# Optimization experiments

Measured on AMD Instinct MI355X. Metric: run time of the kernel, lower is better.

## Reference

```python
import jax, jax.numpy as jnp
import numpy as np

N_NODES = 50000
N_EDGES = 600000
IC, H, OC = 64, 128, 32
EPS = 1e-5


def setup_inputs() -> dict:
    key = jax.random.key(0)
    ks = jax.random.split(key, 8)
    x = jax.random.normal(ks[0], (N_NODES, IC), dtype=jnp.float32)
    ei = jax.random.randint(ks[1], (2, N_EDGES), 0, N_NODES, dtype=jnp.int64)
    proj_w = jax.random.normal(ks[2], (IC, H), dtype=jnp.float32) * 0.05
    proj_b = jnp.zeros((H,), dtype=jnp.float32)
    # conv_w[layer, lin, :, :] with lin order: key, query, value, skip
    conv_w = jax.random.normal(ks[3], (3, 4, H, H), dtype=jnp.float32) * 0.05
    conv_b = jnp.zeros((3, 4, H), dtype=jnp.float32)
    bn_gamma = jnp.ones((3, H), dtype=jnp.float32)
    bn_beta = jnp.zeros((3, H), dtype=jnp.float32)
    head_w = jax.random.normal(ks[4], (H, OC), dtype=jnp.float32) * 0.05
    head_b = jnp.zeros((OC,), dtype=jnp.float32)
    return {"x": x, "ei": ei, "proj_w": proj_w, "proj_b": proj_b,
            "conv_w": conv_w, "conv_b": conv_b, "bn_gamma": bn_gamma,
            "bn_beta": bn_beta, "head_w": head_w, "head_b": head_b}


def _res_gated_conv(x, src, dst, w, b):
    # PyG ResGatedGraphConv: out_i = skip(x_i) + sum_j sigmoid(key(x_i)+query(x_j)) * value(x_j)
    k = x @ w[0] + b[0]      # key   (applied to target/dst)
    q = x @ w[1] + b[1]      # query (applied to source/src)
    v = x @ w[2] + b[2]      # value (applied to source/src)
    msg = jax.nn.sigmoid(k[dst] + q[src]) * v[src]          # [E, H]
    agg = jax.ops.segment_sum(msg, dst, num_segments=x.shape[0])  # [N, H]
    return x @ w[3] + b[3] + agg


def _batchnorm(x, gamma, beta):
    # training-mode BatchNorm1d: batch statistics over the node dimension
    mean = jnp.mean(x, axis=0)
    var = jnp.var(x, axis=0)
    return gamma * (x - mean) * jax.lax.rsqrt(var + EPS) + beta


def reference(x, ei, proj_w, proj_b, conv_w, conv_b, bn_gamma, bn_beta, head_w, head_b):
    src, dst = ei[0], ei[1]
    h = jax.nn.relu(x @ proj_w + proj_b)
    for layer in range(3):
        h = _res_gated_conv(h, src, dst, conv_w[layer], conv_b[layer])
        h = jax.nn.relu(_batchnorm(h, bn_gamma[layer], bn_beta[layer]))
        # dropout(p=0.2) is identity in eval mode
    return h @ head_w + head_b
```

## Files before the change

kernel.cpp:

```cpp
#include <hip/hip_runtime.h>
#include <hip/hip_bf16.h>
#include <math.h>

#define HDIM 128
#define ICDIM 64
#define OCDIM 32
#define BN_EPS 1e-5f
#define NCH 64

typedef __attribute__((ext_vector_type(8))) short bv8;
typedef __attribute__((ext_vector_type(4))) float fv4;

static __device__ __forceinline__ unsigned short f2bf(float v) {
    __hip_bfloat16 t = __float2bfloat16(v);
    return *(unsigned short*)&t;
}
static __device__ __forceinline__ float bflo(unsigned int u) {
    union { unsigned int i; float f; } c; c.i = u << 16; return c.f;
}
static __device__ __forceinline__ float bfhi(unsigned int u) {
    union { unsigned int i; float f; } c; c.i = u & 0xffff0000u; return c.f;
}
static __device__ __forceinline__ unsigned int pack2bf(float a, float b) {
    return (unsigned int)f2bf(a) | ((unsigned int)f2bf(b) << 16);
}

__global__ void wprep_kernel(const float* __restrict__ conv_w,
                             const float* __restrict__ proj_w,
                             __hip_bfloat16* __restrict__ Wt,
                             __hip_bfloat16* __restrict__ Wp) {
    int mat = blockIdx.x;
    if (mat < 12) {
        const float* s = conv_w + (size_t)mat * HDIM * HDIM;
        __hip_bfloat16* d = Wt + (size_t)mat * HDIM * HDIM;
        for (int idx = threadIdx.x; idx < HDIM * HDIM; idx += 256) {
            int i = idx >> 7, o = idx & 127;
            d[(size_t)o * HDIM + i] = __float2bfloat16(s[idx]);
        }
    } else {
        for (int idx = threadIdx.x; idx < ICDIM * HDIM; idx += 256) {
            int i = idx >> 7, o = idx & 127;
            Wp[(size_t)o * ICDIM + i] = __float2bfloat16(proj_w[idx]);
        }
    }
}

__global__ __launch_bounds__(256)
void proj_mfma_kernel(const float* __restrict__ x,
                      const __hip_bfloat16* __restrict__ wp,
                      const float* __restrict__ b,
                      __hip_bfloat16* __restrict__ h, int n) {
    __shared__ unsigned int xs[NCH * ICDIM / 2];
    int tid = threadIdx.x;
    int m0 = blockIdx.x * NCH;

    const float2* xsrc = (const float2*)(x + (size_t)m0 * ICDIM);
    for (int i = tid; i < NCH * ICDIM / 2; i += 256) {
        int node = m0 + (i >> 5);
        float2 v = (node < n) ? xsrc[i] : (float2){0.f, 0.f};
        xs[i ^ (((i >> 5) & 7) << 2)] = pack2bf(v.x, v.y);
    }

    int wv = tid >> 6;
    int lane = tid & 63;
    int j = lane & 15;
    int kg = lane >> 4;
    int sw = (j & 7) << 4;

    bv8 af[2][2];
#pragma unroll
    for (int gs = 0; gs < 2; ++gs)
#pragma unroll
        for (int ks = 0; ks < 2; ++ks)
            af[gs][ks] = *(const bv8*)((const unsigned short*)wp +
                (size_t)(wv * 32 + gs * 16 + j) * ICDIM + ks * 32 + kg * 8);

    float4 bias0 = *(const float4*)(b + wv * 32 + kg * 4);
    float4 bias1 = *(const float4*)(b + wv * 32 + 16 + kg * 4);

    __syncthreads();

#pragma unroll
    for (int t4 = 0; t4 < NCH / 16; ++t4) {
        const char* rowbase = (const char*)xs + (t4 * 16 + j) * (ICDIM * 2);
        fv4 acc0 = (fv4){0.f, 0.f, 0.f, 0.f};
        fv4 acc1 = (fv4){0.f, 0.f, 0.f, 0.f};
#pragma unroll
        for (int ks = 0; ks < 2; ++ks) {
            bv8 bf = *(const bv8*)(rowbase + ((kg * 16 + ks * 64) ^ sw));
            acc0 = __builtin_amdgcn_mfma_f32_16x16x32_bf16(af[0][ks], bf, acc0, 0, 0, 0);
            acc1 = __builtin_amdgcn_mfma_f32_16x16x32_bf16(af[1][ks], bf, acc1, 0, 0, 0);
        }
        int node = m0 + t4 * 16 + j;
        if (node < n) {
            unsigned short* o =
                (unsigned short*)h + (size_t)node * HDIM + wv * 32 + kg * 4;
            ushort4 r0, r1;
            r0.x = f2bf(fmaxf(acc0.x + bias0.x, 0.f));
            r0.y = f2bf(fmaxf(acc0.y + bias0.y, 0.f));
            r0.z = f2bf(fmaxf(acc0.z + bias0.z, 0.f));
            r0.w = f2bf(fmaxf(acc0.w + bias0.w, 0.f));
            r1.x = f2bf(fmaxf(acc1.x + bias1.x, 0.f));
            r1.y = f2bf(fmaxf(acc1.y + bias1.y, 0.f));
            r1.z = f2bf(fmaxf(acc1.z + bias1.z, 0.f));
            r1.w = f2bf(fmaxf(acc1.w + bias1.w, 0.f));
            *(ushort4*)o = r0;
            *(ushort4*)(o + 16) = r1;
        }
    }
}

__global__ __launch_bounds__(1024)
void gemm4_fused_kernel(const __hip_bfloat16* __restrict__ hB,
                        const float* __restrict__ Ssrc,
                        const float* __restrict__ stp,
                        const float* __restrict__ gma,
                        const float* __restrict__ bta,
                        const __hip_bfloat16* __restrict__ wt4,
                        const float* __restrict__ b4,
                        __hip_bfloat16* __restrict__ K,
                        unsigned int* __restrict__ QV,
                        float* __restrict__ S, int n) {
    __shared__ unsigned short hs[NCH * HDIM];
    int tid = threadIdx.x;
    int m0 = blockIdx.x * NCH;
    int wsw = ((tid >> 4) & 7) << 4;

    if (Ssrc) {
        const float4* src = (const float4*)(Ssrc + (size_t)m0 * HDIM);
        float4 v0 = src[tid * 2];
        float4 v1 = src[tid * 2 + 1];
        int c0 = (tid * 8) & 127;
        float invn = 1.f / (float)n;
        float vv[8] = {v0.x, v0.y, v0.z, v0.w, v1.x, v1.y, v1.z, v1.w};
        unsigned int* dst = (unsigned int*)((char*)hs + ((tid * 16) ^ wsw));
#pragma unroll
        for (int p = 0; p < 8; p += 2) {
            int c = c0 + p;
            float mA = stp[c] * invn, mB = stp[c + 1] * invn;
            float scA = gma[c] * rsqrtf(stp[128 + c] * invn - mA * mA + BN_EPS);
            float scB = gma[c + 1] * rsqrtf(stp[129 + c] * invn - mB * mB + BN_EPS);
            float shA = bta[c] - mA * scA, shB = bta[c + 1] - mB * scB;
            float rA = fmaxf(fmaf(vv[p], scA, shA), 0.f);
            float rB = fmaxf(fmaf(vv[p + 1], scB, shB), 0.f);
            dst[p >> 1] = pack2bf(rA, rB);
        }
    } else {
        const uint4* src = (const uint4*)((const unsigned short*)hB + (size_t)m0 * HDIM);
        *(uint4*)((char*)hs + ((tid * 16) ^ wsw)) = src[tid];
    }

    int wv = tid >> 6;
    int lane = tid & 63;
    int lin = wv >> 2;
    int g2 = wv & 3;
    int j = lane & 15;
    int kg = lane >> 4;
    int sw = (j & 7) << 4;

    const unsigned short* wbase =
        (const unsigned short*)(wt4 + (size_t)lin * HDIM * HDIM);
    bv8 af[2][4];
#pragma unroll
    for (int gs = 0; gs < 2; ++gs)
#pragma unroll
        for (int ks = 0; ks < 4; ++ks)
            af[gs][ks] = *(const bv8*)(wbase +
                (size_t)(g2 * 32 + gs * 16 + j) * HDIM + ks * 32 + kg * 8);

    const float* bl = b4 + lin * HDIM;
    float4 bias0 = *(const float4*)(bl + g2 * 32 + kg * 4);
    float4 bias1 = *(const float4*)(bl + g2 * 32 + 16 + kg * 4);

    __syncthreads();

#pragma unroll
    for (int t4 = 0; t4 < NCH / 16; ++t4) {
        const char* rowbase = (const char*)hs + (t4 * 16 + j) * (HDIM * 2);
        fv4 acc0 = (fv4){0.f, 0.f, 0.f, 0.f};
        fv4 acc1 = (fv4){0.f, 0.f, 0.f, 0.f};
#pragma unroll
        for (int ks = 0; ks < 4; ++ks) {
            bv8 bf = *(const bv8*)(rowbase + ((kg * 16 + ks * 64) ^ sw));
            acc0 = __builtin_amdgcn_mfma_f32_16x16x32_bf16(af[0][ks], bf, acc0, 0, 0, 0);
            acc1 = __builtin_amdgcn_mfma_f32_16x16x32_bf16(af[1][ks], bf, acc1, 0, 0, 0);
        }
        int node = m0 + t4 * 16 + j;
        if (node >= n) continue;
        int c0 = g2 * 32 + kg * 4;
        float f0 = acc0.x + bias0.x, f1 = acc0.y + bias0.y;
        float f2 = acc0.z + bias0.z, f3 = acc0.w + bias0.w;
        float f4 = acc1.x + bias1.x, f5 = acc1.y + bias1.y;
        float f6 = acc1.z + bias1.z, f7 = acc1.w + bias1.w;
        if (lin == 3) {
            float* o = S + (size_t)node * HDIM + c0;
            *(float4*)o = (float4){f0, f1, f2, f3};
            *(float4*)(o + 16) = (float4){f4, f5, f6, f7};
        } else if (lin == 0) {
            unsigned short* o = (unsigned short*)K + (size_t)node * HDIM + c0;
            *(ushort4*)o = (ushort4){f2bf(f0), f2bf(f1), f2bf(f2), f2bf(f3)};
            *(ushort4*)(o + 16) = (ushort4){f2bf(f4), f2bf(f5), f2bf(f6), f2bf(f7)};
        } else {
            unsigned short* o = (unsigned short*)QV + (size_t)node * 256 + 2 * c0
                              + ((lin == 2) ? 4 : 0);
            *(ushort4*)o = (ushort4){f2bf(f0), f2bf(f1), f2bf(f2), f2bf(f3)};
            *(ushort4*)(o + 32) = (ushort4){f2bf(f4), f2bf(f5), f2bf(f6), f2bf(f7)};
        }
    }
}

__global__ void hist_kernel(const int* __restrict__ ei, int* __restrict__ deg, int e) {
    int i = blockIdx.x * 256 + threadIdx.x;
    if (i < e) atomicAdd(&deg[ei[(size_t)e + i]], 1);
}

__global__ void scan1_kernel(const int* __restrict__ deg, int* __restrict__ incl,
                             int* __restrict__ bsum, int n) {
    __shared__ int tmp[256];
    int i = blockIdx.x * 256 + threadIdx.x;
    int v = (i < n) ? deg[i] : 0;
    tmp[threadIdx.x] = v;
    __syncthreads();
    for (int ofs = 1; ofs < 256; ofs <<= 1) {
        int t = (threadIdx.x >= ofs) ? tmp[threadIdx.x - ofs] : 0;
        __syncthreads();
        tmp[threadIdx.x] += t;
        __syncthreads();
    }
    if (i < n) incl[i] = tmp[threadIdx.x];
    if (threadIdx.x == 255) bsum[blockIdx.x] = tmp[255];
}

__global__ void scan23_kernel(const int* __restrict__ deg, const int* __restrict__ incl,
                              const int* __restrict__ bsum, int* __restrict__ off,
                              int* __restrict__ cursor, int n, int e, int nb) {
    __shared__ int tmp[256];
    int t = threadIdx.x;
    tmp[t] = (t < nb) ? bsum[t] : 0;
    __syncthreads();
    for (int ofs = 1; ofs < 256; ofs <<= 1) {
        int a = (t >= ofs) ? tmp[t - ofs] : 0;
        __syncthreads();
        tmp[t] += a;
        __syncthreads();
    }
    int pre = (blockIdx.x == 0) ? 0 : tmp[blockIdx.x - 1];
    int i = blockIdx.x * 256 + t;
    if (i < n) {
        int ex = incl[i] - deg[i] + pre;
        off[i] = ex;
        cursor[i] = ex;
        if (i == n - 1) off[n] = e;
    }
}

__global__ void scatter_kernel(const int* __restrict__ ei, int* __restrict__ cursor,
                               int* __restrict__ esrc, int e) {
    int i = blockIdx.x * 256 + threadIdx.x;
    if (i < e) {
        int dst = ei[(size_t)e + i];
        int pos = atomicAdd(&cursor[dst], 1);
        esrc[pos] = ei[i];
    }
}

__global__ void agg_kernel(const int* __restrict__ off, const int* __restrict__ esrc,
                           const __hip_bfloat16* __restrict__ kb,
                           const unsigned int* __restrict__ QV,
                           float* __restrict__ S, int n) {
    int d = blockIdx.x * 4 + (threadIdx.x >> 6);
    if (d >= n) return;
    int lane = threadIdx.x & 63;
    int half = lane >> 5;
    int cl = lane & 31;
    const char* qvb = (const char*)QV;

    uint2 ku = *(const uint2*)((const unsigned short*)kb + (size_t)d * HDIM + 4 * cl);
    float k0 = bflo(ku.x), k1 = bfhi(ku.x), k2 = bflo(ku.y), k3 = bfhi(ku.y);
    float a0 = 0.f, a1 = 0.f, a2 = 0.f, a3 = 0.f;

#define EDGE4(u)                                                     \
    {                                                                \
        float g0 = k0 + bflo(u.x), g1 = k1 + bfhi(u.x);              \
        float g2 = k2 + bflo(u.y), g3 = k3 + bfhi(u.y);              \
        a0 += __fdividef(bflo(u.z), 1.f + __expf(-g0));              \
        a1 += __fdividef(bfhi(u.z), 1.f + __expf(-g1));              \
        a2 += __fdividef(bflo(u.w), 1.f + __expf(-g2));              \
        a3 += __fdividef(bfhi(u.w), 1.f + __expf(-g3));              \
    }

    int j = off[d] + half, s1 = off[d + 1];
    for (; j + 2 < s1; j += 4) {
        int sA = esrc[j], sB = esrc[j + 2];
        uint4 uA = *(const uint4*)(qvb + (size_t)sA * 512 + cl * 16);
        uint4 uB = *(const uint4*)(qvb + (size_t)sB * 512 + cl * 16);
        EDGE4(uA);
        EDGE4(uB);
    }
    if (j < s1) {
        int sA = esrc[j];
        uint4 uA = *(const uint4*)(qvb + (size_t)sA * 512 + cl * 16);
        EDGE4(uA);
    }
#undef EDGE4

    a0 += __shfl_xor(a0, 32);
    a1 += __shfl_xor(a1, 32);
    a2 += __shfl_xor(a2, 32);
    a3 += __shfl_xor(a3, 32);
    if (half == 0) {
        float4* sp = (float4*)(S + (size_t)d * HDIM) + cl;
        float4 o = *sp;
        o.x += a0; o.y += a1; o.z += a2; o.w += a3;
        *sp = o;
    }
}

__global__ void stats_kernel(const float* __restrict__ s,
                             float* __restrict__ stats, int n) {
    int c = threadIdx.x & 127, rh = threadIdx.x >> 7;
    int r0 = blockIdx.x * 128;
    int r1 = min(r0 + 128, n);
    float sum = 0.f, sq = 0.f;
    for (int r = r0 + rh; r < r1; r += 2) {
        float v = s[(size_t)r * HDIM + c];
        sum += v;
        sq = fmaf(v, v, sq);
    }
    __shared__ float ls[2][HDIM], lq[2][HDIM];
    ls[rh][c] = sum;
    lq[rh][c] = sq;
    __syncthreads();
    if (rh == 0) {
        atomicAdd(&stats[c], ls[0][c] + ls[1][c]);
        atomicAdd(&stats[HDIM + c], lq[0][c] + lq[1][c]);
    }
}

__global__ void head_bn_kernel(const float* __restrict__ S,
                               const float* __restrict__ stats,
                               const float* __restrict__ gamma,
                               const float* __restrict__ beta,
                               const float* __restrict__ w,
                               const float* __restrict__ b,
                               float* __restrict__ out, int n) {
    __shared__ float hsm[8][HDIM];
    float invn = 1.f / (float)n;
    for (int i = threadIdx.x; i < 8 * HDIM; i += 256) {
        int r = i >> 7, c = i & 127;
        int node = blockIdx.x * 8 + r;
        float v = 0.f;
        if (node < n) {
            float mean = stats[c] * invn;
            float var = stats[128 + c] * invn - mean * mean;
            float sc = gamma[c] * rsqrtf(var + BN_EPS);
            float sh = beta[c] - mean * sc;
            v = fmaxf(fmaf(S[(size_t)node * HDIM + c], sc, sh), 0.f);
        }
        hsm[r][c] = v;
    }
    __syncthreads();
    int c = threadIdx.x & 31;
    int ng = threadIdx.x >> 5;
    int node = blockIdx.x * 8 + ng;
    if (node >= n) return;
    float acc = b[c];
#pragma unroll
    for (int k = 0; k < HDIM; ++k)
        acc = fmaf(hsm[ng][k], w[k * OCDIM + c], acc);
    out[(size_t)node * OCDIM + c] = acc;
}

extern "C" void kernel_launch(void* const* d_in, const int* in_sizes, int n_in,
                              void* d_out, int out_size, void* d_ws, size_t ws_size,
                              hipStream_t stream) {
    const float* x      = (const float*)d_in[0];
    const int*   ei     = (const int*)  d_in[1];
    const float* proj_w = (const float*)d_in[2];
    const float* proj_b = (const float*)d_in[3];
    const float* conv_w = (const float*)d_in[4];
    const float* conv_b = (const float*)d_in[5];
    const float* bn_g   = (const float*)d_in[6];
    const float* bn_b   = (const float*)d_in[7];
    const float* head_w = (const float*)d_in[8];
    const float* head_b = (const float*)d_in[9];
    float* out = (float*)d_out;

    int n = in_sizes[0] / ICDIM;
    int e = in_sizes[1] / 2;

    size_t nh = (size_t)n * HDIM;
    size_t need = nh * 4 + 768 * 4 + nh * 2 + nh * 2 + nh * 4
                + (size_t)12 * HDIM * HDIM * 2 + (size_t)HDIM * ICDIM * 2
                + ((size_t)3 * n + (n + 1) + 256 + e) * 4;
    if (ws_size < need) return;

    float* S  = (float*)d_ws;
    float* st = S + nh;
    __hip_bfloat16* h = (__hip_bfloat16*)(st + 768);
    __hip_bfloat16* K = h + nh;
    unsigned int* QV = (unsigned int*)(K + nh);
    __hip_bfloat16* Wt = (__hip_bfloat16*)(QV + nh);
    __hip_bfloat16* Wp = Wt + (size_t)12 * HDIM * HDIM;

    int* deg    = (int*)(Wp + (size_t)HDIM * ICDIM);
    int* incl   = deg + n;
    int* off    = incl + n;
    int* cursor = off + n + 1;
    int* bsum   = cursor + n;
    int* esrc   = bsum + 256;

    hipMemsetAsync(st, 0, 768 * sizeof(float), stream);
    hipMemsetAsync(deg, 0, (size_t)n * sizeof(int), stream);

    int gb_e = (e + 255) / 256;
    int gb_n = (n + 255) / 256;

    wprep_kernel<<<13, 256, 0, stream>>>(conv_w, proj_w, Wt, Wp);
    proj_mfma_kernel<<<(n + NCH - 1) / NCH, 256, 0, stream>>>(x, Wp, proj_b, h, n);

    hist_kernel<<<gb_e, 256, 0, stream>>>(ei, deg, e);
    scan1_kernel<<<gb_n, 256, 0, stream>>>(deg, incl, bsum, n);
    scan23_kernel<<<gb_n, 256, 0, stream>>>(deg, incl, bsum, off, cursor, n, e, gb_n);
    scatter_kernel<<<gb_e, 256, 0, stream>>>(ei, cursor, esrc, e);

    int gm = (n + NCH - 1) / NCH;
    for (int l = 0; l < 3; ++l) {
        const float* Ssrc = (l == 0) ? nullptr : S;
        const float* stp  = (l == 0) ? st : st + (size_t)(l - 1) * 256;
        const float* gma  = (l == 0) ? bn_g : bn_g + (size_t)(l - 1) * HDIM;
        const float* bta  = (l == 0) ? bn_b : bn_b + (size_t)(l - 1) * HDIM;
        gemm4_fused_kernel<<<gm, 1024, 0, stream>>>(
            h, Ssrc, stp, gma, bta,
            Wt + (size_t)l * 4 * HDIM * HDIM, conv_b + (size_t)l * 4 * HDIM,
            K, QV, S, n);
        agg_kernel<<<(n + 3) / 4, 256, 0, stream>>>(off, esrc, K, QV, S, n);
        stats_kernel<<<(n + 127) / 128, 256, 0, stream>>>(S, st + l * 256, n);
    }

    head_bn_kernel<<<(n + 7) / 8, 256, 0, stream>>>(
        S, st + 2 * 256, bn_g + 2 * HDIM, bn_b + 2 * HDIM, head_w, head_b, out, n);
}
```

Baseline: 467.8 us.

## Fuse BatchNorm statistics into persistent aggregation kernel and enlarge GEMM node tile

The separate stats kernel is removed. The aggregation kernel becomes grid-stride persistent with 2048 blocks and accumulates per-channel sum and sum-of-squares while writing S, then reduces them in shared memory and issues one atomic per channel per block. This drops a full re-read of S and one launch per layer. The fused GEMM kernel also processes 128 nodes per block instead of 64, which halves the block count and amortizes the per-block weight-fragment loads, at the cost of more shared memory and a longer per-block loop. The tail block of the GEMM now reads its staging rows beyond n, as the 64-node version also did for its last partial tile.

```diff
diff --git a/kernel.cpp b/kernel.cpp
--- a/kernel.cpp
+++ b/kernel.cpp
@@ -7,6 +7,7 @@
 #define OCDIM 32
 #define BN_EPS 1e-5f
 #define NCH 64
+#define NCHG 128
 
 typedef __attribute__((ext_vector_type(8))) short bv8;
 typedef __attribute__((ext_vector_type(4))) float fv4;
@@ -121,33 +122,42 @@
                         __hip_bfloat16* __restrict__ K,
                         unsigned int* __restrict__ QV,
                         float* __restrict__ S, int n) {
-    __shared__ unsigned short hs[NCH * HDIM];
+    __shared__ unsigned short hs[NCHG * HDIM];
     int tid = threadIdx.x;
-    int m0 = blockIdx.x * NCH;
-    int wsw = ((tid >> 4) & 7) << 4;
+    int m0 = blockIdx.x * NCHG;
 
     if (Ssrc) {
         const float4* src = (const float4*)(Ssrc + (size_t)m0 * HDIM);
-        float4 v0 = src[tid * 2];
-        float4 v1 = src[tid * 2 + 1];
-        int c0 = (tid * 8) & 127;
         float invn = 1.f / (float)n;
-        float vv[8] = {v0.x, v0.y, v0.z, v0.w, v1.x, v1.y, v1.z, v1.w};
-        unsigned int* dst = (unsigned int*)((char*)hs + ((tid * 16) ^ wsw));
-#pragma unroll
-        for (int p = 0; p < 8; p += 2) {
-            int c = c0 + p;
-            float mA = stp[c] * invn, mB = stp[c + 1] * invn;
-            float scA = gma[c] * rsqrtf(stp[128 + c] * invn - mA * mA + BN_EPS);
-            float scB = gma[c + 1] * rsqrtf(stp[129 + c] * invn - mB * mB + BN_EPS);
-            float shA = bta[c] - mA * scA, shB = bta[c + 1] - mB * scB;
-            float rA = fmaxf(fmaf(vv[p], scA, shA), 0.f);
-            float rB = fmaxf(fmaf(vv[p + 1], scB, shB), 0.f);
-            dst[p >> 1] = pack2bf(rA, rB);
+#pragma unroll
+        for (int it = 0; it < 2; ++it) {
+            int idx = it * 1024 + tid;
+            float4 v0 = src[idx * 2];
+            float4 v1 = src[idx * 2 + 1];
+            int c0 = (idx * 8) & 127;
+            float vv[8] = {v0.x, v0.y, v0.z, v0.w, v1.x, v1.y, v1.z, v1.w};
+            int wsw = ((idx >> 4) & 7) << 4;
+            unsigned int* dst = (unsigned int*)((char*)hs + ((idx * 16) ^ wsw));
+#pragma unroll
+            for (int p = 0; p < 8; p += 2) {
+                int c = c0 + p;
+                float mA = stp[c] * invn, mB = stp[c + 1] * invn;
+                float scA = gma[c] * rsqrtf(stp[128 + c] * invn - mA * mA + BN_EPS);
+                float scB = gma[c + 1] * rsqrtf(stp[129 + c] * invn - mB * mB + BN_EPS);
+                float shA = bta[c] - mA * scA, shB = bta[c + 1] - mB * scB;
+                float rA = fmaxf(fmaf(vv[p], scA, shA), 0.f);
+                float rB = fmaxf(fmaf(vv[p + 1], scB, shB), 0.f);
+                dst[p >> 1] = pack2bf(rA, rB);
+            }
         }
     } else {
         const uint4* src = (const uint4*)((const unsigned short*)hB + (size_t)m0 * HDIM);
-        *(uint4*)((char*)hs + ((tid * 16) ^ wsw)) = src[tid];
+#pragma unroll
+        for (int it = 0; it < 2; ++it) {
+            int idx = it * 1024 + tid;
+            int wsw = ((idx >> 4) & 7) << 4;
+            *(uint4*)((char*)hs + ((idx * 16) ^ wsw)) = src[idx];
+        }
     }
 
     int wv = tid >> 6;
@@ -175,7 +185,7 @@
     __syncthreads();
 
 #pragma unroll
-    for (int t4 = 0; t4 < NCH / 16; ++t4) {
+    for (int t4 = 0; t4 < NCHG / 16; ++t4) {
         const char* rowbase = (const char*)hs + (t4 * 16 + j) * (HDIM * 2);
         fv4 acc0 = (fv4){0.f, 0.f, 0.f, 0.f};
         fv4 acc1 = (fv4){0.f, 0.f, 0.f, 0.f};
@@ -264,20 +274,19 @@
     }
 }
 
-__global__ void agg_kernel(const int* __restrict__ off, const int* __restrict__ esrc,
-                           const __hip_bfloat16* __restrict__ kb,
-                           const unsigned int* __restrict__ QV,
-                           float* __restrict__ S, int n) {
-    int d = blockIdx.x * 4 + (threadIdx.x >> 6);
-    if (d >= n) return;
+__global__ __launch_bounds__(256)
+void agg_kernel(const int* __restrict__ off, const int* __restrict__ esrc,
+                const __hip_bfloat16* __restrict__ kb,
+                const unsigned int* __restrict__ QV,
+                float* __restrict__ S, float* __restrict__ stats, int n) {
+    int wv = threadIdx.x >> 6;
     int lane = threadIdx.x & 63;
     int half = lane >> 5;
     int cl = lane & 31;
     const char* qvb = (const char*)QV;
 
-    uint2 ku = *(const uint2*)((const unsigned short*)kb + (size_t)d * HDIM + 4 * cl);
-    float k0 = bflo(ku.x), k1 = bfhi(ku.x), k2 = bflo(ku.y), k3 = bfhi(ku.y);
-    float a0 = 0.f, a1 = 0.f, a2 = 0.f, a3 = 0.f;
+    float ss0 = 0.f, ss1 = 0.f, ss2 = 0.f, ss3 = 0.f;
+    float sq0 = 0.f, sq1 = 0.f, sq2 = 0.f, sq3 = 0.f;
 
 #define EDGE4(u)                                                     \
     {                                                                \
@@ -289,52 +298,57 @@
         a3 += __fdividef(bfhi(u.w), 1.f + __expf(-g3));              \
     }
 
-    int j = off[d] + half, s1 = off[d + 1];
-    for (; j + 2 < s1; j += 4) {
-        int sA = esrc[j], sB = esrc[j + 2];
-        uint4 uA = *(const uint4*)(qvb + (size_t)sA * 512 + cl * 16);
-        uint4 uB = *(const uint4*)(qvb + (size_t)sB * 512 + cl * 16);
-        EDGE4(uA);
-        EDGE4(uB);
-    }
-    if (j < s1) {
-        int sA = esrc[j];
-        uint4 uA = *(const uint4*)(qvb + (size_t)sA * 512 + cl * 16);
-        EDGE4(uA);
+    for (int d = blockIdx.x * 4 + wv; d < n; d += gridDim.x * 4) {
+        uint2 ku = *(const uint2*)((const unsigned short*)kb + (size_t)d * HDIM + 4 * cl);
+        float k0 = bflo(ku.x), k1 = bfhi(ku.x), k2 = bflo(ku.y), k3 = bfhi(ku.y);
+        float a0 = 0.f, a1 = 0.f, a2 = 0.f, a3 = 0.f;
+
+        int j = off[d] + half, s1 = off[d + 1];
+        for (; j + 2 < s1; j += 4) {
+            int sA = esrc[j], sB = esrc[j + 2];
+            uint4 uA = *(const uint4*)(qvb + (size_t)sA * 512 + cl * 16);
+            uint4 uB = *(const uint4*)(qvb + (size_t)sB * 512 + cl * 16);
+            EDGE4(uA);
+            EDGE4(uB);
+        }
+        if (j < s1) {
+            int sA = esrc[j];
+            uint4 uA = *(const uint4*)(qvb + (size_t)sA * 512 + cl * 16);
+            EDGE4(uA);
+        }
+
+        a0 += __shfl_xor(a0, 32);
+        a1 += __shfl_xor(a1, 32);
+        a2 += __shfl_xor(a2, 32);
+        a3 += __shfl_xor(a3, 32);
+        if (half == 0) {
+            float4* sp = (float4*)(S + (size_t)d * HDIM) + cl;
+            float4 o = *sp;
+            o.x += a0; o.y += a1; o.z += a2; o.w += a3;
+            *sp = o;
+            ss0 += o.x; sq0 = fmaf(o.x, o.x, sq0);
+            ss1 += o.y; sq1 = fmaf(o.y, o.y, sq1);
+            ss2 += o.z; sq2 = fmaf(o.z, o.z, sq2);
+            ss3 += o.w; sq3 = fmaf(o.w, o.w, sq3);
+        }
     }
 #undef EDGE4
 
-    a0 += __shfl_xor(a0, 32);
-    a1 += __shfl_xor(a1, 32);
-    a2 += __shfl_xor(a2, 32);
-    a3 += __shfl_xor(a3, 32);
+    __shared__ float red[4][256];
     if (half == 0) {
-        float4* sp = (float4*)(S + (size_t)d * HDIM) + cl;
-        float4 o = *sp;
-        o.x += a0; o.y += a1; o.z += a2; o.w += a3;
-        *sp = o;
-    }
-}
-
-__global__ void stats_kernel(const float* __restrict__ s,
-                             float* __restrict__ stats, int n) {
-    int c = threadIdx.x & 127, rh = threadIdx.x >> 7;
-    int r0 = blockIdx.x * 128;
-    int r1 = min(r0 + 128, n);
-    float sum = 0.f, sq = 0.f;
-    for (int r = r0 + rh; r < r1; r += 2) {
-        float v = s[(size_t)r * HDIM + c];
-        sum += v;
-        sq = fmaf(v, v, sq);
-    }
-    __shared__ float ls[2][HDIM], lq[2][HDIM];
-    ls[rh][c] = sum;
-    lq[rh][c] = sq;
-    __syncthreads();
-    if (rh == 0) {
-        atomicAdd(&stats[c], ls[0][c] + ls[1][c]);
-        atomicAdd(&stats[HDIM + c], lq[0][c] + lq[1][c]);
-    }
+        red[wv][cl * 4 + 0] = ss0;
+        red[wv][cl * 4 + 1] = ss1;
+        red[wv][cl * 4 + 2] = ss2;
+        red[wv][cl * 4 + 3] = ss3;
+        red[wv][128 + cl * 4 + 0] = sq0;
+        red[wv][128 + cl * 4 + 1] = sq1;
+        red[wv][128 + cl * 4 + 2] = sq2;
+        red[wv][128 + cl * 4 + 3] = sq3;
+    }
+    __syncthreads();
+    int t = threadIdx.x;
+    float v = red[0][t] + red[1][t] + red[2][t] + red[3][t];
+    atomicAdd(&stats[t], v);
 }
 
 __global__ void head_bn_kernel(const float* __restrict__ S,
@@ -424,7 +438,7 @@
     scan23_kernel<<<gb_n, 256, 0, stream>>>(deg, incl, bsum, off, cursor, n, e, gb_n);
     scatter_kernel<<<gb_e, 256, 0, stream>>>(ei, cursor, esrc, e);
 
-    int gm = (n + NCH - 1) / NCH;
+    int gm = (n + NCHG - 1) / NCHG;
     for (int l = 0; l < 3; ++l) {
         const float* Ssrc = (l == 0) ? nullptr : S;
         const float* stp  = (l == 0) ? st : st + (size_t)(l - 1) * 256;
@@ -434,8 +448,7 @@
             h, Ssrc, stp, gma, bta,
             Wt + (size_t)l * 4 * HDIM * HDIM, conv_b + (size_t)l * 4 * HDIM,
             K, QV, S, n);
-        agg_kernel<<<(n + 3) / 4, 256, 0, stream>>>(off, esrc, K, QV, S, n);
-        stats_kernel<<<(n + 127) / 128, 256, 0, stream>>>(S, st + l * 256, n);
+        agg_kernel<<<2048, 256, 0, stream>>>(off, esrc, K, QV, S, st + l * 256, n);
     }
 
     head_bn_kernel<<<(n + 7) / 8, 256, 0, stream>>>(
```

After: 492.8 us. +5.3%, slower.
